# Performance work log

Measured on AMD Instinct MI355X. Metric: run time of the kernel, lower is better.

Reference implementation:

```python
import jax, jax.numpy as jnp
import numpy as np

N_QUBITS = 12
FAST_DEPTH = 4
FAST_DECAY = 0.9
LATENT = 512
BATCH = 2048


def _apply_ry(state, theta, wire):
    # state: (B, 2**n) real; RY is a real rotation. PennyLane default.qubit:
    # wire 0 is the most-significant bit of the state index.
    B = state.shape[0]
    s = state.reshape(B, 1 << wire, 2, -1)
    h = theta * 0.5
    c = jnp.cos(h)[:, None, None]
    sn = jnp.sin(h)[:, None, None]
    s0, s1 = s[:, :, 0], s[:, :, 1]
    out = jnp.stack([c * s0 - sn * s1, sn * s0 + c * s1], axis=2)
    return out.reshape(state.shape)


def _apply_cnot_adjacent(state, wire):
    # CNOT with control=wire, target=wire+1 (nearest-neighbor chain)
    B = state.shape[0]
    s = state.reshape(B, 1 << wire, 2, 2, -1)
    out = jnp.stack([s[:, :, 0], s[:, :, 1, ::-1]], axis=2)
    return out.reshape(state.shape)


def _fwp_circuit(x, fast, n_qubits, n_outputs):
    # x: (B, n_qubits) RY encoding angles; fast: (B, depth, n_qubits)
    B = x.shape[0]
    dim = 1 << n_qubits
    # Hadamard layer on |0...0> -> uniform positive real amplitudes.
    state = jnp.full((B, dim), 2.0 ** (-n_qubits / 2), dtype=x.dtype)
    for w in range(n_qubits):
        state = _apply_ry(state, x[:, w], w)
    for layer in range(fast.shape[1]):
        for w in range(n_qubits - 1):
            state = _apply_cnot_adjacent(state, w)
        for w in range(n_qubits):
            state = _apply_ry(state, fast[:, layer, w], w)
    probs = state * state  # real state -> |amp|^2
    outs = []
    for w in range(n_outputs):
        p = probs.reshape(B, 1 << w, 2, -1)
        outs.append(p[:, :, 0].sum(axis=(1, 2)) - p[:, :, 1].sum(axis=(1, 2)))
    return jnp.stack(outs, axis=1)  # (B, n_outputs) PauliZ expvals


def setup_inputs() -> dict:
    key = jax.random.key(0)
    ks = jax.random.split(key, 6)
    n, depth, latent = N_QUBITS, FAST_DEPTH, LATENT
    return {
        "x_t": jax.random.normal(ks[0], (BATCH, n), jnp.float32),
        "fast_prev": jax.random.normal(ks[1], (BATCH, depth, n), jnp.float32) * 0.1,
        "W_enc": jax.random.normal(ks[2], (latent, n), jnp.float32) / np.sqrt(n).astype(np.float32),
        "b_enc": jnp.zeros((latent,), jnp.float32),
        "W_upd": jax.random.normal(ks[3], (depth * n, latent), jnp.float32) / np.sqrt(latent).astype(np.float32),
        "b_upd": jnp.zeros((depth * n,), jnp.float32),
        "W_ro": jax.random.normal(ks[4], (1, n), jnp.float32) / np.sqrt(n).astype(np.float32),
        "b_ro": jnp.zeros((1,), jnp.float32),
    }


def reference(x_t, fast_prev, W_enc, b_enc, W_upd, b_upd, W_ro, b_ro):
    latent = jnp.tanh(x_t @ W_enc.T + b_enc)
    delta = (latent @ W_upd.T + b_upd).reshape(x_t.shape[0], FAST_DEPTH, N_QUBITS)
    fast_next = FAST_DECAY * fast_prev + delta
    q_out = _fwp_circuit(x_t, fast_next, N_QUBITS, N_QUBITS)  # n_outputs = n_qubits
    y_t = q_out @ W_ro.T + b_ro
    return (y_t, fast_next)
```

## Files before the change

### kernel.cpp

```cpp
#include <hip/hip_runtime.h>

static constexpr int NQ    = 12;
static constexpr int DEPTH = 4;
static constexpr int LAT   = 512;
static constexpr int FAST  = DEPTH * NQ;
static constexpr float DECAY = 0.9f;
static constexpr int PITCH = 66;

using v2f = __attribute__((ext_vector_type(2))) float;


template<int S, int B>
__device__ __forceinline__ void bfly_half(float (&v)[64], float c, float s) {
    v2f c2 = {c, c}, s2 = {s, s};
    #pragma unroll
    for (int r0 = B; r0 < B + 32; r0 += 2) {
        if ((r0 & S) == 0) {
            v2f a = {v[r0],     v[r0 + 1]};
            v2f b = {v[r0 + S], v[r0 + S + 1]};
            v2f na = c2 * a - s2 * b;
            v2f nb = s2 * a + c2 * b;
            v[r0]         = na.x;  v[r0 + 1]     = na.y;
            v[r0 + S]     = nb.x;  v[r0 + S + 1] = nb.y;
        }
    }
}

template<int B>
__device__ __forceinline__ void bfly1_half(float (&v)[64], float c, float s) {
    v2f cs = {c, s}, nsc = {-s, c};
    #pragma unroll
    for (int r0 = B; r0 < B + 32; r0 += 2) {
        float a = v[r0], b = v[r0 + 1];
        v2f aa = {a, a}, bb = {b, b};
        v2f res = cs * aa + nsc * bb;
        v[r0]     = res.x;
        v[r0 + 1] = res.y;
    }
}

template<int B>
__device__ __forceinline__ void ry5_half(float (&v)[64], const float* c, const float* s) {
    bfly_half<16, B>(v, c[0], s[0]);
    bfly_half<8,  B>(v, c[1], s[1]);
    bfly_half<4,  B>(v, c[2], s[2]);
    bfly_half<2,  B>(v, c[3], s[3]);
    bfly1_half<B>(v, c[4], s[4]);
}

__device__ __forceinline__ void bfly32(float (&v)[64], float c, float s) {
    v2f c2 = {c, c}, s2 = {s, s};
    #pragma unroll
    for (int r0 = 0; r0 < 32; r0 += 2) {
        v2f a = {v[r0],      v[r0 + 1]};
        v2f b = {v[r0 + 32], v[r0 + 33]};
        v2f na = c2 * a - s2 * b;
        v2f nb = s2 * a + c2 * b;
        v[r0]      = na.x;  v[r0 + 1]  = na.y;
        v[r0 + 32] = nb.x;  v[r0 + 33] = nb.y;
    }
}

__global__ __launch_bounds__(64, 2)
void fwp_kernel(const float* __restrict__ x_t,
                const float* __restrict__ fast_prev,
                const float* __restrict__ W_enc,
                const float* __restrict__ b_enc,
                const float* __restrict__ W_upd,
                const float* __restrict__ b_upd,
                const float* __restrict__ W_ro,
                const float* __restrict__ b_ro,
                float* __restrict__ out_y,
                float* __restrict__ out_fast) {
    const int lane = threadIdx.x;
    const int b    = blockIdx.x;

    __shared__ __align__(16) float s_xch[64 * PITCH];
    __shared__ float s_c[FAST], s_s[FAST];

    float* s_lat = s_xch;

    const float* xrow = x_t + b * NQ;
    float xa[NQ];
    #pragma unroll
    for (int k = 0; k < NQ; k++) xa[k] = xrow[k];

    #pragma unroll
    for (int t = 0; t < LAT / 64; t++) {
        int j = lane + 64 * t;
        const float4* wr = (const float4*)(W_enc + j * NQ);
        float4 a0 = wr[0], a1 = wr[1], a2 = wr[2];
        float sum = b_enc[j]
            + a0.x * xa[0] + a0.y * xa[1] + a0.z * xa[2]  + a0.w * xa[3]
            + a1.x * xa[4] + a1.y * xa[5] + a1.z * xa[6]  + a1.w * xa[7]
            + a2.x * xa[8] + a2.y * xa[9] + a2.z * xa[10] + a2.w * xa[11];
        s_lat[j] = tanhf(sum);
    }

    if (lane < FAST) {
        const float4* wr = (const float4*)(W_upd + lane * LAT);
        const float4* lr = (const float4*)(s_lat);
        float sum = b_upd[lane];
        #pragma unroll 16
        for (int j = 0; j < LAT / 4; j++) {
            float4 w4 = wr[j];
            float4 l4 = lr[j];
            sum += w4.x * l4.x + w4.y * l4.y + w4.z * l4.z + w4.w * l4.w;
        }
        float ang = DECAY * fast_prev[b * FAST + lane] + sum;
        out_fast[b * FAST + lane] = ang;
        float hh = 0.5f * ang;
        s_c[lane] = __cosf(hh);
        s_s[lane] = __sinf(hh);
    }

    float g0[NQ], g1[NQ];
    #pragma unroll
    for (int w = 0; w < NQ; w++) {
        float hh = 0.5f * xa[w];
        float c = __cosf(hh), s = __sinf(hh);
        g0[w] = (c - s) * 0.70710678118654752f;
        g1[w] = (c + s) * 0.70710678118654752f;
    }
    float L = 1.0f;
    #pragma unroll
    for (int w = 0; w < 6; w++)
        L *= ((lane >> (5 - w)) & 1) ? g1[w] : g0[w];

    float v[64];
    v[0] = L;
    #pragma unroll
    for (int w = 6; w < NQ; w++) {
        const int S = 1 << (11 - w);
        #pragma unroll
        for (int r = 0; r < 64; r += 2 * S) {
            v[r + S] = v[r] * g1[w];
            v[r]     = v[r] * g0[w];
        }
    }

    const int A0 = ((lane ^ (lane >> 1)) & 31) | (lane & 32);
    const int A1 = A0 ^ 32;

    #pragma unroll
    for (int layer = 0; layer < DEPTH; layer++) {
        float lc[NQ], ls[NQ];
        #pragma unroll
        for (int w = 0; w < NQ; w++) {
            lc[w] = s_c[layer * NQ + w];
            ls[w] = s_s[layer * NQ + w];
        }

        #pragma unroll
        for (int k = 0; k < 32; k++)
            *(v2f*)&s_xch[lane * PITCH + 2 * k] = (v2f){v[2 * k], v[2 * k + 1]};
        #pragma unroll
        for (int r = 0; r < 32; r++) {
            const int g = r ^ (r >> 1);
            v[r] = s_xch[g * PITCH + ((r & 1) ? A1 : A0)];
        }
        ry5_half<0>(v, lc + 1, ls + 1);
        #pragma unroll
        for (int r = 32; r < 64; r++) {
            const int g = r ^ (r >> 1);
            v[r] = s_xch[g * PITCH + ((r & 1) ? A1 : A0)];
        }
        ry5_half<32>(v, lc + 1, ls + 1);
        bfly32(v, lc[0], ls[0]);

        #pragma unroll
        for (int k = 0; k < 32; k++)
            *(v2f*)&s_xch[lane * PITCH + 2 * k] = (v2f){v[2 * k], v[2 * k + 1]};
        #pragma unroll
        for (int r = 0; r < 32; r++) v[r] = s_xch[r * PITCH + lane];
        ry5_half<0>(v, lc + 7, ls + 7);
        #pragma unroll
        for (int r = 32; r < 64; r++) v[r] = s_xch[r * PITCH + lane];
        ry5_half<32>(v, lc + 7, ls + 7);
        bfly32(v, lc[6], ls[6]);
    }

    float tot = 0.0f, pw[6] = {0, 0, 0, 0, 0, 0};
    #pragma unroll
    for (int r = 0; r < 64; r++) {
        float p = v[r] * v[r];
        tot += p;
        pw[0] += (r & 32) ? -p : p;
        pw[1] += (r & 16) ? -p : p;
        pw[2] += (r & 8)  ? -p : p;
        pw[3] += (r & 4)  ? -p : p;
        pw[4] += (r & 2)  ? -p : p;
        pw[5] += (r & 1)  ? -p : p;
    }
    float sl = 0.0f;
    #pragma unroll
    for (int w = 0; w < 6; w++) {
        float c = W_ro[w];
        sl += ((lane >> (5 - w)) & 1) ? -c : c;
    }
    float y = sl * tot;
    #pragma unroll
    for (int k = 0; k < 6; k++) y += W_ro[6 + k] * pw[k];
    #pragma unroll
    for (int m = 32; m >= 1; m >>= 1) y += __shfl_xor(y, m, 64);
    if (lane == 0) out_y[b] = y + b_ro[0];
}

extern "C" void kernel_launch(void* const* d_in, const int* in_sizes, int n_in,
                              void* d_out, int out_size, void* d_ws, size_t ws_size,
                              hipStream_t stream) {
    const float* x_t       = (const float*)d_in[0];
    const float* fast_prev = (const float*)d_in[1];
    const float* W_enc     = (const float*)d_in[2];
    const float* b_enc     = (const float*)d_in[3];
    const float* W_upd     = (const float*)d_in[4];
    const float* b_upd     = (const float*)d_in[5];
    const float* W_ro      = (const float*)d_in[6];
    const float* b_ro      = (const float*)d_in[7];
    float* out = (float*)d_out;

    fwp_kernel<<<2048, 64, 0, stream>>>(x_t, fast_prev, W_enc, b_enc,
                                        W_upd, b_upd, W_ro, b_ro,
                                        out , out + 2048 );
}
```

Measured before the change: 111.8 us.

## Process two batch elements per wavefront and interleave their circuit stages

Each 64-lane block now handles two batch rows, sharing W_enc/W_upd loads across both and interleaving the LDS exchange of one state with the butterfly arithmetic of the other. The goal is to hide LDS transpose latency and amortise the weight reads, with the grid halved to 1024 blocks. In exchange, register pressure doubles (two 64-float state vectors), launch bounds drop to 1 wave per EU minimum, the layer loop is no longer unrolled, and there is less total parallelism, which risks spills or lower occupancy.

```diff
diff --git a/kernel.cpp b/kernel.cpp
--- a/kernel.cpp
+++ b/kernel.cpp
@@ -20,8 +20,8 @@
             v2f b = {v[r0 + S], v[r0 + S + 1]};
             v2f na = c2 * a - s2 * b;
             v2f nb = s2 * a + c2 * b;
-            v[r0]         = na.x;  v[r0 + 1]     = na.y;
-            v[r0 + S]     = nb.x;  v[r0 + S + 1] = nb.y;
+            v[r0]     = na.x;  v[r0 + 1]     = na.y;
+            v[r0 + S] = nb.x;  v[r0 + S + 1] = nb.y;
         }
     }
 }
@@ -61,7 +61,51 @@
     }
 }
 
-__global__ __launch_bounds__(64, 2)
+__device__ __forceinline__ void xw(const float (&v)[64], float* s_xch, int lane) {
+    #pragma unroll
+    for (int k = 0; k < 32; k++)
+        *(v2f*)&s_xch[lane * PITCH + 2 * k] = (v2f){v[2 * k], v[2 * k + 1]};
+}
+
+__device__ __forceinline__ void p1r(float (&v)[64], const float* s_xch, int A0, int A1) {
+    #pragma unroll
+    for (int r = 0; r < 64; r++) {
+        const int g = r ^ (r >> 1);
+        v[r] = s_xch[g * PITCH + ((r & 1) ? A1 : A0)];
+    }
+}
+
+__device__ __forceinline__ void p2r(float (&v)[64], const float* s_xch, int lane) {
+    #pragma unroll
+    for (int r = 0; r < 64; r++) v[r] = s_xch[r * PITCH + lane];
+}
+
+__device__ __forceinline__ void init_state(float (&v)[64], const float (&xa)[NQ], int lane) {
+    float g0[NQ], g1[NQ];
+    #pragma unroll
+    for (int w = 0; w < NQ; w++) {
+        float hh = 0.5f * xa[w];
+        float c = __cosf(hh), s = __sinf(hh);
+        g0[w] = (c - s) * 0.70710678118654752f;
+        g1[w] = (c + s) * 0.70710678118654752f;
+    }
+    float L = 1.0f;
+    #pragma unroll
+    for (int w = 0; w < 6; w++)
+        L *= ((lane >> (5 - w)) & 1) ? g1[w] : g0[w];
+    v[0] = L;
+    #pragma unroll
+    for (int w = 6; w < NQ; w++) {
+        const int S = 1 << (11 - w);
+        #pragma unroll
+        for (int r = 0; r < 64; r += 2 * S) {
+            v[r + S] = v[r] * g1[w];
+            v[r]     = v[r] * g0[w];
+        }
+    }
+}
+
+__global__ __launch_bounds__(64, 1)
 void fwp_kernel(const float* __restrict__ x_t,
                 const float* __restrict__ fast_prev,
                 const float* __restrict__ W_enc,
@@ -73,137 +117,140 @@
                 float* __restrict__ out_y,
                 float* __restrict__ out_fast) {
     const int lane = threadIdx.x;
-    const int b    = blockIdx.x;
+    const int eA   = 2 * blockIdx.x;
+    const int eB   = eA + 1;
 
     __shared__ __align__(16) float s_xch[64 * PITCH];
-    __shared__ float s_c[FAST], s_s[FAST];
-
-    float* s_lat = s_xch;
-
-    const float* xrow = x_t + b * NQ;
-    float xa[NQ];
-    #pragma unroll
-    for (int k = 0; k < NQ; k++) xa[k] = xrow[k];
+    __shared__ __align__(8)  float s_csA[2 * FAST], s_csB[2 * FAST];
+
+    float* s_latA = s_xch;
+    float* s_latB = s_xch + LAT;
+
+    float xaA[NQ], xaB[NQ];
+    #pragma unroll
+    for (int k = 0; k < NQ; k++) {
+        xaA[k] = x_t[eA * NQ + k];
+        xaB[k] = x_t[eB * NQ + k];
+    }
 
     #pragma unroll
     for (int t = 0; t < LAT / 64; t++) {
         int j = lane + 64 * t;
         const float4* wr = (const float4*)(W_enc + j * NQ);
         float4 a0 = wr[0], a1 = wr[1], a2 = wr[2];
-        float sum = b_enc[j]
-            + a0.x * xa[0] + a0.y * xa[1] + a0.z * xa[2]  + a0.w * xa[3]
-            + a1.x * xa[4] + a1.y * xa[5] + a1.z * xa[6]  + a1.w * xa[7]
-            + a2.x * xa[8] + a2.y * xa[9] + a2.z * xa[10] + a2.w * xa[11];
-        s_lat[j] = tanhf(sum);
+        float be = b_enc[j];
+        float sA = be
+            + a0.x * xaA[0] + a0.y * xaA[1] + a0.z * xaA[2]  + a0.w * xaA[3]
+            + a1.x * xaA[4] + a1.y * xaA[5] + a1.z * xaA[6]  + a1.w * xaA[7]
+            + a2.x * xaA[8] + a2.y * xaA[9] + a2.z * xaA[10] + a2.w * xaA[11];
+        float sB = be
+            + a0.x * xaB[0] + a0.y * xaB[1] + a0.z * xaB[2]  + a0.w * xaB[3]
+            + a1.x * xaB[4] + a1.y * xaB[5] + a1.z * xaB[6]  + a1.w * xaB[7]
+            + a2.x * xaB[8] + a2.y * xaB[9] + a2.z * xaB[10] + a2.w * xaB[11];
+        s_latA[j] = tanhf(sA);
+        s_latB[j] = tanhf(sB);
     }
 
     if (lane < FAST) {
         const float4* wr = (const float4*)(W_upd + lane * LAT);
-        const float4* lr = (const float4*)(s_lat);
-        float sum = b_upd[lane];
-        #pragma unroll 16
+        const float4* la = (const float4*)(s_latA);
+        const float4* lb = (const float4*)(s_latB);
+        float sA = b_upd[lane], sB = sA;
+        #pragma unroll 8
         for (int j = 0; j < LAT / 4; j++) {
             float4 w4 = wr[j];
-            float4 l4 = lr[j];
-            sum += w4.x * l4.x + w4.y * l4.y + w4.z * l4.z + w4.w * l4.w;
-        }
-        float ang = DECAY * fast_prev[b * FAST + lane] + sum;
-        out_fast[b * FAST + lane] = ang;
-        float hh = 0.5f * ang;
-        s_c[lane] = __cosf(hh);
-        s_s[lane] = __sinf(hh);
-    }
-
-    float g0[NQ], g1[NQ];
-    #pragma unroll
-    for (int w = 0; w < NQ; w++) {
-        float hh = 0.5f * xa[w];
-        float c = __cosf(hh), s = __sinf(hh);
-        g0[w] = (c - s) * 0.70710678118654752f;
-        g1[w] = (c + s) * 0.70710678118654752f;
-    }
-    float L = 1.0f;
-    #pragma unroll
-    for (int w = 0; w < 6; w++)
-        L *= ((lane >> (5 - w)) & 1) ? g1[w] : g0[w];
-
-    float v[64];
-    v[0] = L;
-    #pragma unroll
-    for (int w = 6; w < NQ; w++) {
-        const int S = 1 << (11 - w);
-        #pragma unroll
-        for (int r = 0; r < 64; r += 2 * S) {
-            v[r + S] = v[r] * g1[w];
-            v[r]     = v[r] * g0[w];
-        }
-    }
+            float4 a4 = la[j];
+            float4 b4 = lb[j];
+            sA += w4.x * a4.x + w4.y * a4.y + w4.z * a4.z + w4.w * a4.w;
+            sB += w4.x * b4.x + w4.y * b4.y + w4.z * b4.z + w4.w * b4.w;
+        }
+        float angA = DECAY * fast_prev[eA * FAST + lane] + sA;
+        float angB = DECAY * fast_prev[eB * FAST + lane] + sB;
+        out_fast[eA * FAST + lane] = angA;
+        out_fast[eB * FAST + lane] = angB;
+        *(v2f*)&s_csA[2 * lane] = (v2f){__cosf(0.5f * angA), __sinf(0.5f * angA)};
+        *(v2f*)&s_csB[2 * lane] = (v2f){__cosf(0.5f * angB), __sinf(0.5f * angB)};
+    }
+
+    float vA[64], vB[64];
+    init_state(vA, xaA, lane);
+    init_state(vB, xaB, lane);
 
     const int A0 = ((lane ^ (lane >> 1)) & 31) | (lane & 32);
     const int A1 = A0 ^ 32;
 
-    #pragma unroll
+    #pragma unroll 1
     for (int layer = 0; layer < DEPTH; layer++) {
-        float lc[NQ], ls[NQ];
+        float lcA[NQ], lsA[NQ], lcB[NQ], lsB[NQ];
         #pragma unroll
         for (int w = 0; w < NQ; w++) {
-            lc[w] = s_c[layer * NQ + w];
-            ls[w] = s_s[layer * NQ + w];
-        }
-
-        #pragma unroll
-        for (int k = 0; k < 32; k++)
-            *(v2f*)&s_xch[lane * PITCH + 2 * k] = (v2f){v[2 * k], v[2 * k + 1]};
-        #pragma unroll
-        for (int r = 0; r < 32; r++) {
-            const int g = r ^ (r >> 1);
-            v[r] = s_xch[g * PITCH + ((r & 1) ? A1 : A0)];
-        }
-        ry5_half<0>(v, lc + 1, ls + 1);
-        #pragma unroll
-        for (int r = 32; r < 64; r++) {
-            const int g = r ^ (r >> 1);
-            v[r] = s_xch[g * PITCH + ((r & 1) ? A1 : A0)];
-        }
-        ry5_half<32>(v, lc + 1, ls + 1);
-        bfly32(v, lc[0], ls[0]);
-
-        #pragma unroll
-        for (int k = 0; k < 32; k++)
-            *(v2f*)&s_xch[lane * PITCH + 2 * k] = (v2f){v[2 * k], v[2 * k + 1]};
-        #pragma unroll
-        for (int r = 0; r < 32; r++) v[r] = s_xch[r * PITCH + lane];
-        ry5_half<0>(v, lc + 7, ls + 7);
-        #pragma unroll
-        for (int r = 32; r < 64; r++) v[r] = s_xch[r * PITCH + lane];
-        ry5_half<32>(v, lc + 7, ls + 7);
-        bfly32(v, lc[6], ls[6]);
-    }
-
-    float tot = 0.0f, pw[6] = {0, 0, 0, 0, 0, 0};
+            v2f ca = *(const v2f*)&s_csA[2 * (layer * NQ + w)];
+            v2f cb = *(const v2f*)&s_csB[2 * (layer * NQ + w)];
+            lcA[w] = ca.x;  lsA[w] = ca.y;
+            lcB[w] = cb.x;  lsB[w] = cb.y;
+        }
+
+        xw(vA, s_xch, lane);
+        p1r(vA, s_xch, A0, A1);
+        xw(vB, s_xch, lane);
+        ry5_half<0>(vA, lcA + 1, lsA + 1);
+        p1r(vB, s_xch, A0, A1);
+        ry5_half<32>(vA, lcA + 1, lsA + 1);
+        bfly32(vA, lcA[0], lsA[0]);
+        ry5_half<0>(vB, lcB + 1, lsB + 1);
+
+        xw(vA, s_xch, lane);
+        ry5_half<32>(vB, lcB + 1, lsB + 1);
+        bfly32(vB, lcB[0], lsB[0]);
+        p2r(vA, s_xch, lane);
+        xw(vB, s_xch, lane);
+        ry5_half<0>(vA, lcA + 7, lsA + 7);
+        p2r(vB, s_xch, lane);
+        ry5_half<32>(vA, lcA + 7, lsA + 7);
+        bfly32(vA, lcA[6], lsA[6]);
+        ry5_half<0>(vB, lcB + 7, lsB + 7);
+        ry5_half<32>(vB, lcB + 7, lsB + 7);
+        bfly32(vB, lcB[6], lsB[6]);
+    }
+
+    float wro[NQ];
+    #pragma unroll
+    for (int w = 0; w < NQ; w++) wro[w] = W_ro[w];
+    float sl = 0.0f;
+    #pragma unroll
+    for (int w = 0; w < 6; w++)
+        sl += ((lane >> (5 - w)) & 1) ? -wro[w] : wro[w];
+
+    float totA = 0.0f, pwA[6] = {0,0,0,0,0,0};
+    float totB = 0.0f, pwB[6] = {0,0,0,0,0,0};
     #pragma unroll
     for (int r = 0; r < 64; r++) {
-        float p = v[r] * v[r];
-        tot += p;
-        pw[0] += (r & 32) ? -p : p;
-        pw[1] += (r & 16) ? -p : p;
-        pw[2] += (r & 8)  ? -p : p;
-        pw[3] += (r & 4)  ? -p : p;
-        pw[4] += (r & 2)  ? -p : p;
-        pw[5] += (r & 1)  ? -p : p;
-    }
-    float sl = 0.0f;
-    #pragma unroll
-    for (int w = 0; w < 6; w++) {
-        float c = W_ro[w];
-        sl += ((lane >> (5 - w)) & 1) ? -c : c;
-    }
-    float y = sl * tot;
-    #pragma unroll
-    for (int k = 0; k < 6; k++) y += W_ro[6 + k] * pw[k];
-    #pragma unroll
-    for (int m = 32; m >= 1; m >>= 1) y += __shfl_xor(y, m, 64);
-    if (lane == 0) out_y[b] = y + b_ro[0];
+        float pA = vA[r] * vA[r];
+        float pB = vB[r] * vB[r];
+        totA += pA;  totB += pB;
+        pwA[0] += (r & 32) ? -pA : pA;  pwB[0] += (r & 32) ? -pB : pB;
+        pwA[1] += (r & 16) ? -pA : pA;  pwB[1] += (r & 16) ? -pB : pB;
+        pwA[2] += (r & 8)  ? -pA : pA;  pwB[2] += (r & 8)  ? -pB : pB;
+        pwA[3] += (r & 4)  ? -pA : pA;  pwB[3] += (r & 4)  ? -pB : pB;
+        pwA[4] += (r & 2)  ? -pA : pA;  pwB[4] += (r & 2)  ? -pB : pB;
+        pwA[5] += (r & 1)  ? -pA : pA;  pwB[5] += (r & 1)  ? -pB : pB;
+    }
+    float yA = sl * totA, yB = sl * totB;
+    #pragma unroll
+    for (int k = 0; k < 6; k++) {
+        yA += wro[6 + k] * pwA[k];
+        yB += wro[6 + k] * pwB[k];
+    }
+    #pragma unroll
+    for (int m = 32; m >= 1; m >>= 1) {
+        yA += __shfl_xor(yA, m, 64);
+        yB += __shfl_xor(yB, m, 64);
+    }
+    if (lane == 0) {
+        float br = b_ro[0];
+        out_y[eA] = yA + br;
+        out_y[eB] = yB + br;
+    }
 }
 
 extern "C" void kernel_launch(void* const* d_in, const int* in_sizes, int n_in,
@@ -219,7 +266,7 @@
     const float* b_ro      = (const float*)d_in[7];
     float* out = (float*)d_out;
 
-    fwp_kernel<<<2048, 64, 0, stream>>>(x_t, fast_prev, W_enc, b_enc,
+    fwp_kernel<<<1024, 64, 0, stream>>>(x_t, fast_prev, W_enc, b_enc,
                                         W_upd, b_upd, W_ro, b_ro,
                                         out , out + 2048 );
 }
```

New measurement: 108.3 us. -3.1%, faster.

## Interleave cos/sin in shared memory, stagger block starts, relax launch bounds

Applied to the files above, without the earlier changes.

Stores each gate's cos and sin as one interleaved float2 in shared memory, so every wire's coefficients come from a single 8-byte LDS read instead of two scalar reads. Adds a per-block s_sleep stagger keyed on blockIdx mod 4, meant to spread out simultaneous global weight loads across blocks. Relaxes launch_bounds min-blocks from 2 to 1, which gives the compiler more register room but may reduce occupancy. The sleep adds idle cycles to three of every four blocks.

```diff
diff --git a/kernel.cpp b/kernel.cpp
--- a/kernel.cpp
+++ b/kernel.cpp
@@ -20,8 +20,8 @@
             v2f b = {v[r0 + S], v[r0 + S + 1]};
             v2f na = c2 * a - s2 * b;
             v2f nb = s2 * a + c2 * b;
-            v[r0]         = na.x;  v[r0 + 1]     = na.y;
-            v[r0 + S]     = nb.x;  v[r0 + S + 1] = nb.y;
+            v[r0]     = na.x;  v[r0 + 1]     = na.y;
+            v[r0 + S] = nb.x;  v[r0 + S + 1] = nb.y;
         }
     }
 }
@@ -40,12 +40,12 @@
 }
 
 template<int B>
-__device__ __forceinline__ void ry5_half(float (&v)[64], const float* c, const float* s) {
-    bfly_half<16, B>(v, c[0], s[0]);
-    bfly_half<8,  B>(v, c[1], s[1]);
-    bfly_half<4,  B>(v, c[2], s[2]);
-    bfly_half<2,  B>(v, c[3], s[3]);
-    bfly1_half<B>(v, c[4], s[4]);
+__device__ __forceinline__ void ry5_half(float (&v)[64], const v2f* cs) {
+    bfly_half<16, B>(v, cs[0].x, cs[0].y);
+    bfly_half<8,  B>(v, cs[1].x, cs[1].y);
+    bfly_half<4,  B>(v, cs[2].x, cs[2].y);
+    bfly_half<2,  B>(v, cs[3].x, cs[3].y);
+    bfly1_half<B>(v, cs[4].x, cs[4].y);
 }
 
 __device__ __forceinline__ void bfly32(float (&v)[64], float c, float s) {
@@ -61,7 +61,7 @@
     }
 }
 
-__global__ __launch_bounds__(64, 2)
+__global__ __launch_bounds__(64, 1)
 void fwp_kernel(const float* __restrict__ x_t,
                 const float* __restrict__ fast_prev,
                 const float* __restrict__ W_enc,
@@ -76,9 +76,16 @@
     const int b    = blockIdx.x;
 
     __shared__ __align__(16) float s_xch[64 * PITCH];
-    __shared__ float s_c[FAST], s_s[FAST];
+    __shared__ __align__(8)  v2f   s_cs[FAST];
 
     float* s_lat = s_xch;
+
+    {
+        const int ph = b & 3;
+        if (ph > 0) __builtin_amdgcn_s_sleep(7);
+        if (ph > 1) __builtin_amdgcn_s_sleep(7);
+        if (ph > 2) __builtin_amdgcn_s_sleep(7);
+    }
 
     const float* xrow = x_t + b * NQ;
     float xa[NQ];
@@ -110,8 +117,7 @@
         float ang = DECAY * fast_prev[b * FAST + lane] + sum;
         out_fast[b * FAST + lane] = ang;
         float hh = 0.5f * ang;
-        s_c[lane] = __cosf(hh);
-        s_s[lane] = __sinf(hh);
+        s_cs[lane] = (v2f){__cosf(hh), __sinf(hh)};
     }
 
     float g0[NQ], g1[NQ];
@@ -144,12 +150,9 @@
 
     #pragma unroll
     for (int layer = 0; layer < DEPTH; layer++) {
-        float lc[NQ], ls[NQ];
-        #pragma unroll
-        for (int w = 0; w < NQ; w++) {
-            lc[w] = s_c[layer * NQ + w];
-            ls[w] = s_s[layer * NQ + w];
-        }
+        v2f cs[NQ];
+        #pragma unroll
+        for (int w = 0; w < NQ; w++) cs[w] = s_cs[layer * NQ + w];
 
         #pragma unroll
         for (int k = 0; k < 32; k++)
@@ -159,25 +162,25 @@
             const int g = r ^ (r >> 1);
             v[r] = s_xch[g * PITCH + ((r & 1) ? A1 : A0)];
         }
-        ry5_half<0>(v, lc + 1, ls + 1);
+        ry5_half<0>(v, cs + 1);
         #pragma unroll
         for (int r = 32; r < 64; r++) {
             const int g = r ^ (r >> 1);
             v[r] = s_xch[g * PITCH + ((r & 1) ? A1 : A0)];
         }
-        ry5_half<32>(v, lc + 1, ls + 1);
-        bfly32(v, lc[0], ls[0]);
+        ry5_half<32>(v, cs + 1);
+        bfly32(v, cs[0].x, cs[0].y);
 
         #pragma unroll
         for (int k = 0; k < 32; k++)
             *(v2f*)&s_xch[lane * PITCH + 2 * k] = (v2f){v[2 * k], v[2 * k + 1]};
         #pragma unroll
         for (int r = 0; r < 32; r++) v[r] = s_xch[r * PITCH + lane];
-        ry5_half<0>(v, lc + 7, ls + 7);
+        ry5_half<0>(v, cs + 7);
         #pragma unroll
         for (int r = 32; r < 64; r++) v[r] = s_xch[r * PITCH + lane];
-        ry5_half<32>(v, lc + 7, ls + 7);
-        bfly32(v, lc[6], ls[6]);
+        ry5_half<32>(v, cs + 7);
+        bfly32(v, cs[6].x, cs[6].y);
     }
 
     float tot = 0.0f, pw[6] = {0, 0, 0, 0, 0, 0};
```

Measured after the change: 112.3 us. About the same (+0.4%).
